# Kernel optimization log

Hardware: AMD Instinct MI355X
Metric: run time of the kernel (lower is better)

Reference implementation:

```python
import jax, jax.numpy as jnp
import numpy as np

N = 50000   # nodes
E = 800000  # edges (avg degree 16)
D = 256     # input = hidden = output dim
L = 3       # num_layers


def setup_inputs() -> dict:
    key = jax.random.key(0)
    k0, k1, k2, k3 = jax.random.split(key, 4)
    x = jax.random.normal(k0, (N, D), dtype=jnp.float32)
    edge_index = jax.random.randint(k1, (2, E), 0, N, dtype=jnp.int32)
    # SAGEConv params per layer: lin_l (neighbor path, with bias), lin_r (root path)
    Wl = jax.random.normal(k2, (L, D, D), dtype=jnp.float32) * 0.05
    Wr = jax.random.normal(k3, (L, D, D), dtype=jnp.float32) * 0.05
    b = jnp.zeros((L, D), dtype=jnp.float32)
    return {"x": x, "edge_index": edge_index, "Wl": Wl, "Wr": Wr, "b": b}


def reference(x, edge_index, Wl, Wr, b):
    src = edge_index[0]
    dst = edge_index[1]
    # in-degree for mean aggregation (clamped to avoid div-by-zero)
    deg = jax.ops.segment_sum(jnp.ones((E,), x.dtype), dst, num_segments=N)
    inv_deg = (1.0 / jnp.maximum(deg, 1.0))[:, None]  # [N,1]
    h = x
    for i in range(L):
        # gather source features, scatter-add into destinations, then mean
        agg = jax.ops.segment_sum(h[src], dst, num_segments=N) * inv_deg  # [N,D]
        h = agg @ Wl[i] + h @ Wr[i] + b[i]
        if i < L - 1:
            h = jax.nn.relu(h)  # dropout(p=0.1) is identity in eval mode
    return h
```

## Files before the change

### kernel.cpp

```cpp
#include <hip/hip_runtime.h>


typedef __attribute__((ext_vector_type(8))) _Float16 f16x8;
typedef __attribute__((ext_vector_type(4))) float f32x4;

__global__ void count_deg_kernel(const int* __restrict__ dst,
                                 int* __restrict__ deg, int E) {
    int e = blockIdx.x * blockDim.x + threadIdx.x;
    if (e < E) atomicAdd(&deg[dst[e]], 1);
}

__device__ __forceinline__ int block_excl_scan_256(int v, int tid) {
    int lane = tid & 63, w = tid >> 6;
    int x = v;
#pragma unroll
    for (int off = 1; off < 64; off <<= 1) {
        int y = __shfl_up(x, off);
        if (lane >= off) x += y;
    }
    __shared__ int wsum[4], woff[4];
    if (lane == 63) wsum[w] = x;
    __syncthreads();
    if (tid == 0) {
        int a = 0;
#pragma unroll
        for (int i = 0; i < 4; ++i) { woff[i] = a; a += wsum[i]; }
    }
    __syncthreads();
    return woff[w] + x - v;
}

__global__ void scan_phase1(const int* __restrict__ deg,
                            int* __restrict__ partial, int n) {
    int base = blockIdx.x * 1024;
    int s = 0;
    for (int i = threadIdx.x; i < 1024; i += 256) {
        int idx = base + i;
        s += (idx < n) ? deg[idx] : 0;
    }
    __shared__ int ws4[4];
    int lane = threadIdx.x & 63, w = threadIdx.x >> 6;
#pragma unroll
    for (int off = 32; off; off >>= 1) s += __shfl_down(s, off);
    if (lane == 0) ws4[w] = s;
    __syncthreads();
    if (threadIdx.x == 0)
        partial[blockIdx.x] = ws4[0] + ws4[1] + ws4[2] + ws4[3];
}

__global__ void scan_phase2(int* __restrict__ partial, int nb,
                            int* __restrict__ rowptr, int n, int E) {
    int tid = threadIdx.x;
    int v = (tid < nb) ? partial[tid] : 0;
    int ex = block_excl_scan_256(v, tid);
    if (tid < nb) partial[tid] = ex;
    if (tid == 0) rowptr[n] = E;
}

__global__ void scan_phase3(const int* __restrict__ deg,
                            const int* __restrict__ partial,
                            int* __restrict__ rowptr, int* __restrict__ cursor,
                            float* __restrict__ inv_deg, int n) {
    int base = blockIdx.x * 1024 + threadIdx.x * 4;
    int d[4];
#pragma unroll
    for (int j = 0; j < 4; ++j) {
        int idx = base + j;
        d[j] = (idx < n) ? deg[idx] : 0;
    }
    int tsum = d[0] + d[1] + d[2] + d[3];
    int ex = block_excl_scan_256(tsum, threadIdx.x);
    int run = partial[blockIdx.x] + ex;
#pragma unroll
    for (int j = 0; j < 4; ++j) {
        int idx = base + j;
        if (idx < n) {
            rowptr[idx] = run;
            cursor[idx] = run;
            inv_deg[idx] = 1.0f / (float)max(d[j], 1);
        }
        run += d[j];
    }
}

__global__ void fill_csr_kernel(const int* __restrict__ src,
                                const int* __restrict__ dst,
                                int* __restrict__ cursor,
                                int* __restrict__ csr_src, int E) {
    int e = blockIdx.x * blockDim.x + threadIdx.x;
    if (e < E) {
        int d = dst[e];
        int pos = atomicAdd(&cursor[d], 1);
        csr_src[pos] = src[e];
    }
}

__global__ void presplit_w_kernel(const float* __restrict__ Wl,
                                  const float* __restrict__ Wr,
                                  _Float16* __restrict__ Wf, int total) {
    int idx = blockIdx.x * blockDim.x + threadIdx.x;
    if (idx >= total) return;
    int l = idx >> 17;
    int rem = idx & 131071;
    int s = rem >> 16;
    int kc = rem & 65535;
    int k = kc >> 8, c = kc & 255;
    const float* W = s ? Wr : Wl;
    float w = W[((size_t)l * 256 + k) * 256 + c];
    int k0c = k >> 5, g = (k >> 3) & 3, j = k & 7;
    int tile = c >> 4, col = c & 15;
    int fi = (l * 2 + s) * 65536 + k0c * 8192 + ((tile * 4 + g) * 16 + col) * 8 + j;
    Wf[fi] = (_Float16)w;
}

__device__ __forceinline__ void gemm_from_lds8(
    const _Float16 (*Ah)[65][8], int tid, const _Float16* __restrict__ Wf_l,
    const float* __restrict__ bias, _Float16* __restrict__ zl,
    _Float16* __restrict__ zr, int r0, int M) {
    const int wave = tid >> 6, lane = tid & 63;
    const int l15 = lane & 15, lg = lane >> 4;
    const int wr = (wave & 1) * 32;
    const int wc = (wave >> 1) * 64;

    f32x4 accl[2][4], accr[2][4];
#pragma unroll
    for (int rt = 0; rt < 2; ++rt)
#pragma unroll
        for (int t = 0; t < 4; ++t) {
            accl[rt][t] = (f32x4)(0.0f);
            accr[rt][t] = (f32x4)(0.0f);
        }

#pragma unroll
    for (int k0 = 0; k0 < 256; k0 += 32) {
        f16x8 a0 = *(const f16x8*)&Ah[(k0 >> 3) + lg][wr + l15][0];
        f16x8 a1 = *(const f16x8*)&Ah[(k0 >> 3) + lg][wr + 16 + l15][0];
        const _Float16* wb = Wf_l + (k0 >> 5) * 8192 + (lg * 16 + l15) * 8;
#pragma unroll
        for (int t = 0; t < 4; ++t) {
            int tg = (wc >> 4) + t;
            f16x8 bl = *(const f16x8*)&wb[tg * 512];
            f16x8 br = *(const f16x8*)&wb[65536 + tg * 512];
            accl[0][t] = __builtin_amdgcn_mfma_f32_16x16x32_f16(a0, bl,
                                                                accl[0][t], 0, 0, 0);
            accl[1][t] = __builtin_amdgcn_mfma_f32_16x16x32_f16(a1, bl,
                                                                accl[1][t], 0, 0, 0);
            accr[0][t] = __builtin_amdgcn_mfma_f32_16x16x32_f16(a0, br,
                                                                accr[0][t], 0, 0, 0);
            accr[1][t] = __builtin_amdgcn_mfma_f32_16x16x32_f16(a1, br,
                                                                accr[1][t], 0, 0, 0);
        }
    }

    float bv[4];
#pragma unroll
    for (int t = 0; t < 4; ++t) bv[t] = bias[wc + t * 16 + l15];
#pragma unroll
    for (int rt = 0; rt < 2; ++rt) {
#pragma unroll
        for (int r = 0; r < 4; ++r) {
            int grow = r0 + wr + rt * 16 + lg * 4 + r;
            if (grow >= M) continue;
#pragma unroll
            for (int t = 0; t < 4; ++t) {
                int col = wc + t * 16 + l15;
                zl[(size_t)grow * 256 + col] = (_Float16)accl[rt][t][r];
                zr[(size_t)grow * 256 + col] =
                    (_Float16)(accr[rt][t][r] + bv[t]);
            }
        }
    }
}

__global__ __launch_bounds__(512) void gemm0_kernel(
    const float* __restrict__ xsrc, _Float16* __restrict__ zl,
    _Float16* __restrict__ zr, const _Float16* __restrict__ Wf_l,
    const float* __restrict__ bias, int M) {
    __shared__ __align__(16) _Float16 Ah[32][65][8];
    const int tid = threadIdx.x;
    const int r0 = blockIdx.x * 64;
#pragma unroll
    for (int i = 0; i < 4; ++i) {
        int idx = i * 512 + tid;
        int row = idx >> 5, g = idx & 31;
        int grow = r0 + row;
        f16x8 v = (f16x8)(_Float16)0;
        if (grow < M) {
            const float4* p = (const float4*)&xsrc[(size_t)grow * 256 + g * 8];
            float4 v0 = p[0], v1 = p[1];
            v[0] = (_Float16)v0.x; v[1] = (_Float16)v0.y;
            v[2] = (_Float16)v0.z; v[3] = (_Float16)v0.w;
            v[4] = (_Float16)v1.x; v[5] = (_Float16)v1.y;
            v[6] = (_Float16)v1.z; v[7] = (_Float16)v1.w;
        }
        *(f16x8*)&Ah[g][row][0] = v;
    }
    __syncthreads();
    gemm_from_lds8(Ah, tid, Wf_l, bias, zl, zr, r0, M);
}

__global__ __launch_bounds__(512) void fused_layer_kernel(
    const _Float16* __restrict__ zl_in, const _Float16* __restrict__ zr_in,
    _Float16* __restrict__ zl_out, _Float16* __restrict__ zr_out,
    const int* __restrict__ rowptr, const int* __restrict__ csr_src,
    const float* __restrict__ inv_deg, const _Float16* __restrict__ Wf_l,
    const float* __restrict__ bias, int M) {
    __shared__ __align__(16) _Float16 Ah[32][65][8];
    const int tid = threadIdx.x;
    const int hw = tid >> 5, li = tid & 31;
    const int r0 = blockIdx.x * 64;

#pragma unroll
    for (int i = 0; i < 4; ++i) {
        int row = hw * 4 + i;
        int v = r0 + row;
        f16x8 hv = (f16x8)(_Float16)0;
        if (v < M) {
            int beg = rowptr[v], end = rowptr[v + 1];
            float acc[8] = {0.f, 0.f, 0.f, 0.f, 0.f, 0.f, 0.f, 0.f};
            int e = beg;
            for (; e + 4 <= end; e += 4) {
                int u0 = csr_src[e], u1 = csr_src[e + 1];
                int u2 = csr_src[e + 2], u3 = csr_src[e + 3];
                f16x8 t0 = *(const f16x8*)&zl_in[(size_t)u0 * 256 + li * 8];
                f16x8 t1 = *(const f16x8*)&zl_in[(size_t)u1 * 256 + li * 8];
                f16x8 t2 = *(const f16x8*)&zl_in[(size_t)u2 * 256 + li * 8];
                f16x8 t3 = *(const f16x8*)&zl_in[(size_t)u3 * 256 + li * 8];
#pragma unroll
                for (int j = 0; j < 8; ++j)
                    acc[j] += ((float)t0[j] + (float)t1[j]) +
                              ((float)t2[j] + (float)t3[j]);
            }
            for (; e < end; ++e) {
                int u = csr_src[e];
                f16x8 t = *(const f16x8*)&zl_in[(size_t)u * 256 + li * 8];
#pragma unroll
                for (int j = 0; j < 8; ++j) acc[j] += (float)t[j];
            }
            float sc = inv_deg[v];
            f16x8 zp = *(const f16x8*)&zr_in[(size_t)v * 256 + li * 8];
#pragma unroll
            for (int j = 0; j < 8; ++j)
                hv[j] = (_Float16)fmaxf(acc[j] * sc + (float)zp[j], 0.0f);
        }
        *(f16x8*)&Ah[li][row][0] = hv;
    }
    __syncthreads();
    gemm_from_lds8(Ah, tid, Wf_l, bias, zl_out, zr_out, r0, M);
}

__global__ void combine_final_kernel(const _Float16* __restrict__ zl,
                                     const _Float16* __restrict__ zr,
                                     const int* __restrict__ rowptr,
                                     const int* __restrict__ csr_src,
                                     const float* __restrict__ inv_deg,
                                     float* __restrict__ fout, int n) {
    int hw = threadIdx.x >> 5, li = threadIdx.x & 31;
    int v = blockIdx.x * 8 + hw;
    if (v >= n) return;
    int beg = rowptr[v], end = rowptr[v + 1];
    float acc[8] = {0.f, 0.f, 0.f, 0.f, 0.f, 0.f, 0.f, 0.f};
    int e = beg;
    for (; e + 4 <= end; e += 4) {
        int u0 = csr_src[e], u1 = csr_src[e + 1];
        int u2 = csr_src[e + 2], u3 = csr_src[e + 3];
        f16x8 t0 = *(const f16x8*)&zl[(size_t)u0 * 256 + li * 8];
        f16x8 t1 = *(const f16x8*)&zl[(size_t)u1 * 256 + li * 8];
        f16x8 t2 = *(const f16x8*)&zl[(size_t)u2 * 256 + li * 8];
        f16x8 t3 = *(const f16x8*)&zl[(size_t)u3 * 256 + li * 8];
#pragma unroll
        for (int j = 0; j < 8; ++j)
            acc[j] += ((float)t0[j] + (float)t1[j]) +
                      ((float)t2[j] + (float)t3[j]);
    }
    for (; e < end; ++e) {
        int u = csr_src[e];
        f16x8 t = *(const f16x8*)&zl[(size_t)u * 256 + li * 8];
#pragma unroll
        for (int j = 0; j < 8; ++j) acc[j] += (float)t[j];
    }
    float sc = inv_deg[v];
    f16x8 zp = *(const f16x8*)&zr[(size_t)v * 256 + li * 8];
    float o[8];
#pragma unroll
    for (int j = 0; j < 8; ++j) o[j] = acc[j] * sc + (float)zp[j];
    float4* op = (float4*)&fout[(size_t)v * 256 + li * 8];
    op[0] = make_float4(o[0], o[1], o[2], o[3]);
    op[1] = make_float4(o[4], o[5], o[6], o[7]);
}

extern "C" void kernel_launch(void* const* d_in, const int* in_sizes, int n_in,
                              void* d_out, int out_size, void* d_ws, size_t ws_size,
                              hipStream_t stream) {
    const int D = 256;
    const int N = in_sizes[0] / D;
    const int E = in_sizes[1] / 2;
    const int L = in_sizes[2] / (D * D);

    const float* x  = (const float*)d_in[0];
    const int*   ei = (const int*)d_in[1];
    const float* Wl = (const float*)d_in[2];
    const float* Wr = (const float*)d_in[3];
    const float* b  = (const float*)d_in[4];
    const int* src = ei;
    const int* dst = ei + E;

    size_t off = 0;
    auto alloc = [&](size_t bytes) {
        void* p = (char*)d_ws + off;
        off += (bytes + 255) & ~(size_t)255;
        return p;
    };
    int*   deg     = (int*)alloc((size_t)N * 4);
    int*   rowptr  = (int*)alloc((size_t)(N + 1) * 4);
    int*   cursor  = (int*)alloc((size_t)N * 4);
    float* inv_deg = (float*)alloc((size_t)N * 4);
    int*   csr_src = (int*)alloc((size_t)E * 4);
    int*   partial = (int*)alloc(256 * 4);
    _Float16* zlA = (_Float16*)alloc((size_t)N * D * 2);
    _Float16* zrA = (_Float16*)alloc((size_t)N * D * 2);
    _Float16* Wf  = (_Float16*)alloc((size_t)L * 2 * 65536 * 2);
    (void)ws_size;

    _Float16* zlB = (_Float16*)d_out;
    _Float16* zrB = zlB + (size_t)N * D;
    float* outf = (float*)d_out;

    const int scan_blocks = (N + 1023) / 1024;

    hipMemsetAsync(deg, 0, (size_t)N * 4, stream);
    hipLaunchKernelGGL(count_deg_kernel, dim3((E + 255) / 256), dim3(256), 0,
                       stream, dst, deg, E);
    hipLaunchKernelGGL(scan_phase1, dim3(scan_blocks), dim3(256), 0, stream,
                       deg, partial, N);
    hipLaunchKernelGGL(scan_phase2, dim3(1), dim3(256), 0, stream,
                       partial, scan_blocks, rowptr, N, E);
    hipLaunchKernelGGL(scan_phase3, dim3(scan_blocks), dim3(256), 0, stream,
                       deg, partial, rowptr, cursor, inv_deg, N);
    hipLaunchKernelGGL(fill_csr_kernel, dim3((E + 255) / 256), dim3(256), 0,
                       stream, src, dst, cursor, csr_src, E);

    int wtotal = L * 2 * 65536;
    hipLaunchKernelGGL(presplit_w_kernel, dim3((wtotal + 255) / 256), dim3(256),
                       0, stream, Wl, Wr, Wf, wtotal);

    const int gemm_blocks = (N + 63) / 64;
    const int comb_blocks = (N + 7) / 8;

    hipLaunchKernelGGL(gemm0_kernel, dim3(gemm_blocks), dim3(512), 0, stream,
                       x, zlA, zrA, Wf, b, N);
    hipLaunchKernelGGL(fused_layer_kernel, dim3(gemm_blocks), dim3(512), 0,
                       stream, zlA, zrA, zlB, zrB, rowptr, csr_src, inv_deg,
                       Wf + 131072, b + D, N);
    hipLaunchKernelGGL(fused_layer_kernel, dim3(gemm_blocks), dim3(512), 0,
                       stream, zlB, zrB, zlA, zrA, rowptr, csr_src, inv_deg,
                       Wf + 262144, b + 2 * D, N);
    hipLaunchKernelGGL(combine_final_kernel, dim3(comb_blocks), dim3(256), 0,
                       stream, zlA, zrA, rowptr, csr_src, inv_deg, outf, N);
}
```

Baseline: 379.4 us.

## Halve fused-layer row tile to 32 and issue eight gathers per batch

The fused aggregate+GEMM layer kernel now handles 32 rows per block instead of 64. It uses a new 32-row MFMA GEMM helper, so twice as many blocks launch, which should give more parallelism and latency hiding for the neighbor gathers. The gather loops in the fused and final combine kernels now issue eight neighbor loads per batch, with clamped indices and predicated accumulation, replacing the unroll-by-4 loop plus tail. Each weight fragment is now reused across fewer rows, so the weight traffic per row doubles. The clamped loads also fetch redundant rows on the last partial batch.

```diff
diff --git a/kernel.cpp b/kernel.cpp
--- a/kernel.cpp
+++ b/kernel.cpp
@@ -113,7 +113,7 @@
     Wf[fi] = (_Float16)w;
 }
 
-__device__ __forceinline__ void gemm_from_lds8(
+__device__ __forceinline__ void gemm_from_lds64(
     const _Float16 (*Ah)[65][8], int tid, const _Float16* __restrict__ Wf_l,
     const float* __restrict__ bias, _Float16* __restrict__ zl,
     _Float16* __restrict__ zr, int r0, int M) {
@@ -172,6 +172,54 @@
     }
 }
 
+__device__ __forceinline__ void gemm_from_lds32(
+    const _Float16 (*Ah)[33][8], int tid, const _Float16* __restrict__ Wf_l,
+    const float* __restrict__ bias, _Float16* __restrict__ zl,
+    _Float16* __restrict__ zr, int r0, int M) {
+    const int wave = tid >> 6, lane = tid & 63;
+    const int l15 = lane & 15, lg = lane >> 4;
+    const int wr = (wave & 1) * 16;
+    const int wc = (wave >> 1) * 64;
+
+    f32x4 accl[4], accr[4];
+#pragma unroll
+    for (int t = 0; t < 4; ++t) {
+        accl[t] = (f32x4)(0.0f);
+        accr[t] = (f32x4)(0.0f);
+    }
+
+#pragma unroll
+    for (int k0 = 0; k0 < 256; k0 += 32) {
+        f16x8 a = *(const f16x8*)&Ah[(k0 >> 3) + lg][wr + l15][0];
+        const _Float16* wb = Wf_l + (k0 >> 5) * 8192 + (lg * 16 + l15) * 8;
+#pragma unroll
+        for (int t = 0; t < 4; ++t) {
+            int tg = (wc >> 4) + t;
+            f16x8 bl = *(const f16x8*)&wb[tg * 512];
+            f16x8 br = *(const f16x8*)&wb[65536 + tg * 512];
+            accl[t] = __builtin_amdgcn_mfma_f32_16x16x32_f16(a, bl, accl[t],
+                                                             0, 0, 0);
+            accr[t] = __builtin_amdgcn_mfma_f32_16x16x32_f16(a, br, accr[t],
+                                                             0, 0, 0);
+        }
+    }
+
+    float bv[4];
+#pragma unroll
+    for (int t = 0; t < 4; ++t) bv[t] = bias[wc + t * 16 + l15];
+#pragma unroll
+    for (int r = 0; r < 4; ++r) {
+        int grow = r0 + wr + lg * 4 + r;
+        if (grow >= M) continue;
+#pragma unroll
+        for (int t = 0; t < 4; ++t) {
+            int col = wc + t * 16 + l15;
+            zl[(size_t)grow * 256 + col] = (_Float16)accl[t][r];
+            zr[(size_t)grow * 256 + col] = (_Float16)(accr[t][r] + bv[t]);
+        }
+    }
+}
+
 __global__ __launch_bounds__(512) void gemm0_kernel(
     const float* __restrict__ xsrc, _Float16* __restrict__ zl,
     _Float16* __restrict__ zr, const _Float16* __restrict__ Wf_l,
@@ -196,7 +244,7 @@
         *(f16x8*)&Ah[g][row][0] = v;
     }
     __syncthreads();
-    gemm_from_lds8(Ah, tid, Wf_l, bias, zl, zr, r0, M);
+    gemm_from_lds64(Ah, tid, Wf_l, bias, zl, zr, r0, M);
 }
 
 __global__ __launch_bounds__(512) void fused_layer_kernel(
@@ -205,37 +253,34 @@
     const int* __restrict__ rowptr, const int* __restrict__ csr_src,
     const float* __restrict__ inv_deg, const _Float16* __restrict__ Wf_l,
     const float* __restrict__ bias, int M) {
-    __shared__ __align__(16) _Float16 Ah[32][65][8];
+    __shared__ __align__(16) _Float16 Ah[32][33][8];
     const int tid = threadIdx.x;
     const int hw = tid >> 5, li = tid & 31;
-    const int r0 = blockIdx.x * 64;
-
-#pragma unroll
-    for (int i = 0; i < 4; ++i) {
-        int row = hw * 4 + i;
+    const int r0 = blockIdx.x * 32;
+
+#pragma unroll
+    for (int i = 0; i < 2; ++i) {
+        int row = hw * 2 + i;
         int v = r0 + row;
         f16x8 hv = (f16x8)(_Float16)0;
         if (v < M) {
             int beg = rowptr[v], end = rowptr[v + 1];
             float acc[8] = {0.f, 0.f, 0.f, 0.f, 0.f, 0.f, 0.f, 0.f};
-            int e = beg;
-            for (; e + 4 <= end; e += 4) {
-                int u0 = csr_src[e], u1 = csr_src[e + 1];
-                int u2 = csr_src[e + 2], u3 = csr_src[e + 3];
-                f16x8 t0 = *(const f16x8*)&zl_in[(size_t)u0 * 256 + li * 8];
-                f16x8 t1 = *(const f16x8*)&zl_in[(size_t)u1 * 256 + li * 8];
-                f16x8 t2 = *(const f16x8*)&zl_in[(size_t)u2 * 256 + li * 8];
-                f16x8 t3 = *(const f16x8*)&zl_in[(size_t)u3 * 256 + li * 8];
-#pragma unroll
-                for (int j = 0; j < 8; ++j)
-                    acc[j] += ((float)t0[j] + (float)t1[j]) +
-                              ((float)t2[j] + (float)t3[j]);
-            }
-            for (; e < end; ++e) {
-                int u = csr_src[e];
-                f16x8 t = *(const f16x8*)&zl_in[(size_t)u * 256 + li * 8];
-#pragma unroll
-                for (int j = 0; j < 8; ++j) acc[j] += (float)t[j];
+            for (int e = beg; e < end; e += 8) {
+                f16x8 t[8];
+#pragma unroll
+                for (int k = 0; k < 8; ++k) {
+                    int ee = min(e + k, end - 1);
+                    int u = csr_src[ee];
+                    t[k] = *(const f16x8*)&zl_in[(size_t)u * 256 + li * 8];
+                }
+#pragma unroll
+                for (int k = 0; k < 8; ++k) {
+                    if (e + k < end) {
+#pragma unroll
+                        for (int j = 0; j < 8; ++j) acc[j] += (float)t[k][j];
+                    }
+                }
             }
             float sc = inv_deg[v];
             f16x8 zp = *(const f16x8*)&zr_in[(size_t)v * 256 + li * 8];
@@ -246,7 +291,7 @@
         *(f16x8*)&Ah[li][row][0] = hv;
     }
     __syncthreads();
-    gemm_from_lds8(Ah, tid, Wf_l, bias, zl_out, zr_out, r0, M);
+    gemm_from_lds32(Ah, tid, Wf_l, bias, zl_out, zr_out, r0, M);
 }
 
 __global__ void combine_final_kernel(const _Float16* __restrict__ zl,
@@ -260,24 +305,21 @@
     if (v >= n) return;
     int beg = rowptr[v], end = rowptr[v + 1];
     float acc[8] = {0.f, 0.f, 0.f, 0.f, 0.f, 0.f, 0.f, 0.f};
-    int e = beg;
-    for (; e + 4 <= end; e += 4) {
-        int u0 = csr_src[e], u1 = csr_src[e + 1];
-        int u2 = csr_src[e + 2], u3 = csr_src[e + 3];
-        f16x8 t0 = *(const f16x8*)&zl[(size_t)u0 * 256 + li * 8];
-        f16x8 t1 = *(const f16x8*)&zl[(size_t)u1 * 256 + li * 8];
-        f16x8 t2 = *(const f16x8*)&zl[(size_t)u2 * 256 + li * 8];
-        f16x8 t3 = *(const f16x8*)&zl[(size_t)u3 * 256 + li * 8];
-#pragma unroll
-        for (int j = 0; j < 8; ++j)
-            acc[j] += ((float)t0[j] + (float)t1[j]) +
-                      ((float)t2[j] + (float)t3[j]);
-    }
-    for (; e < end; ++e) {
-        int u = csr_src[e];
-        f16x8 t = *(const f16x8*)&zl[(size_t)u * 256 + li * 8];
-#pragma unroll
-        for (int j = 0; j < 8; ++j) acc[j] += (float)t[j];
+    for (int e = beg; e < end; e += 8) {
+        f16x8 t[8];
+#pragma unroll
+        for (int k = 0; k < 8; ++k) {
+            int ee = min(e + k, end - 1);
+            int u = csr_src[ee];
+            t[k] = *(const f16x8*)&zl[(size_t)u * 256 + li * 8];
+        }
+#pragma unroll
+        for (int k = 0; k < 8; ++k) {
+            if (e + k < end) {
+#pragma unroll
+                for (int j = 0; j < 8; ++j) acc[j] += (float)t[k][j];
+            }
+        }
     }
     float sc = inv_deg[v];
     f16x8 zp = *(const f16x8*)&zr[(size_t)v * 256 + li * 8];
@@ -344,15 +386,16 @@
     hipLaunchKernelGGL(presplit_w_kernel, dim3((wtotal + 255) / 256), dim3(256),
                        0, stream, Wl, Wr, Wf, wtotal);
 
-    const int gemm_blocks = (N + 63) / 64;
+    const int gemm0_blocks = (N + 63) / 64;
+    const int fused_blocks = (N + 31) / 32;
     const int comb_blocks = (N + 7) / 8;
 
-    hipLaunchKernelGGL(gemm0_kernel, dim3(gemm_blocks), dim3(512), 0, stream,
+    hipLaunchKernelGGL(gemm0_kernel, dim3(gemm0_blocks), dim3(512), 0, stream,
                        x, zlA, zrA, Wf, b, N);
-    hipLaunchKernelGGL(fused_layer_kernel, dim3(gemm_blocks), dim3(512), 0,
+    hipLaunchKernelGGL(fused_layer_kernel, dim3(fused_blocks), dim3(512), 0,
                        stream, zlA, zrA, zlB, zrB, rowptr, csr_src, inv_deg,
                        Wf + 131072, b + D, N);
-    hipLaunchKernelGGL(fused_layer_kernel, dim3(gemm_blocks), dim3(512), 0,
+    hipLaunchKernelGGL(fused_layer_kernel, dim3(fused_blocks), dim3(512), 0,
                        stream, zlB, zrB, zlA, zrA, rowptr, csr_src, inv_deg,
                        Wf + 262144, b + 2 * D, N);
     hipLaunchKernelGGL(combine_final_kernel, dim3(comb_blocks), dim3(256), 0,
```

New measurement: 389.6 us. +2.7%, slower.
